# Kernel tuning notes

Hardware: AMD Instinct MI355X
Metric: run time of the kernel (lower is better)

Reference implementation:

```python
import jax, jax.numpy as jnp
import numpy as np

EPS = 1e-05  # epsilon from __init__
K, D = 2048, 256  # codebook_size, embed dim (hardcoded in module)
B, T = 8, 8192


def setup_inputs() -> dict:
    key = jax.random.key(0)
    k1, k2, k3 = jax.random.split(key, 3)
    hidden_states = jax.random.normal(k1, (B, T, D), dtype=jnp.float32)
    embed_sum = jax.random.normal(k2, (K, D), dtype=jnp.float32)
    # cluster_usage starts as ones in the module; use positive random counts
    cluster_usage = jax.random.uniform(k3, (K,), dtype=jnp.float32) * 10.0 + 0.5
    return {"hidden_states": hidden_states, "embed_sum": embed_sum, "cluster_usage": cluster_usage}


def reference(hidden_states, embed_sum, cluster_usage):
    # embed property: embed_sum / clamp(cluster_usage, min=eps)[:, None]
    embed = embed_sum / jnp.clip(cluster_usage, EPS, None)[:, None]  # [K, D]

    shape = hidden_states.shape
    x = hidden_states.reshape(-1, shape[-1]).astype(jnp.float32)  # [N, D]

    x2 = jnp.sum(x * x, axis=-1, keepdims=True)        # [N, 1]
    e2 = jnp.sum(embed * embed, axis=-1)               # [K]
    d2 = x2 - 2.0 * (x @ embed.T) + e2[None, :]        # [N, K] -- the big intermediate

    embed_ind = jnp.argmin(d2, axis=-1).reshape(shape[:-1])  # [B, T]
    # decode: embedding lookup of selected codes
    quantized = jnp.take(embed, embed_ind, axis=0)            # [B, T, D]
    return embed_ind, quantized
```

## Files before the change

### kernel.cpp

```cpp
#include <hip/hip_runtime.h>
#include <hip/hip_bf16.h>


typedef float f32x4 __attribute__((ext_vector_type(4)));
typedef short s16x8 __attribute__((ext_vector_type(8)));
typedef _Float16 h16x8 __attribute__((ext_vector_type(8)));

#define D_DIM 256
#define N_ROWS 65536
#define K_CODES 2048
#define VQ_EPS 1e-5f
#define DELTA 0.25f

__device__ __forceinline__ short f16s(float f) {
    _Float16 h = (_Float16)f;
    return __builtin_bit_cast(short, h);
}
__device__ __forceinline__ unsigned fkey(float f) {
    unsigned u = __float_as_uint(f);
    return u ^ (unsigned)(((int)u >> 31) | (int)0x80000000);
}
__device__ __forceinline__ float funkey(unsigned k) {
    unsigned u = (k & 0x80000000u) ? (k ^ 0x80000000u) : ~k;
    return __uint_as_float(u);
}
__device__ __forceinline__ void gload16(const void* g, void* l) {
    __builtin_amdgcn_global_load_lds(
        (const __attribute__((address_space(1))) void*)g,
        (__attribute__((address_space(3))) void*)l, 16, 0, 0);
}

__device__ __forceinline__ void np_sumsq_16lane(const float* a, float* out, int g) {
#pragma clang fp contract(off)
    int j = g & 7, h = g >> 3;
    const float* p = a + h * 128;
    float t = p[j];
    float r = t * t;
#pragma unroll
    for (int i = 1; i < 16; ++i) { float v = p[j + 8 * i]; r += v * v; }
    r += __shfl_xor(r, 1);
    r += __shfl_xor(r, 2);
    r += __shfl_xor(r, 4);
    float other = __shfl_xor(r, 8);
    if (g == 0) *out = r + other;
}

__global__ void prep_codebook(const float* __restrict__ es, const float* __restrict__ us,
                              float* __restrict__ embed, unsigned short* __restrict__ eswz,
                              float* __restrict__ e2) {
    __shared__ float le[8][256];
    const int tid = threadIdx.x;
    const int rloc = tid >> 5, idx = tid & 31;
    const int r = blockIdx.x * 8 + rloc;
    const float u = fmaxf(us[r], VQ_EPS);
    f32x4 v0 = *(const f32x4*)&es[r * D_DIM + idx * 8];
    f32x4 v1 = *(const f32x4*)&es[r * D_DIM + idx * 8 + 4];
    f32x4 e0, e1;
#pragma unroll
    for (int j = 0; j < 4; ++j) { e0[j] = v0[j] / u; e1[j] = v1[j] / u; }
    *(f32x4*)&embed[r * D_DIM + idx * 8] = e0;
    *(f32x4*)&embed[r * D_DIM + idx * 8 + 4] = e1;
    *(f32x4*)&le[rloc][idx * 8] = e0;
    *(f32x4*)&le[rloc][idx * 8 + 4] = e1;
    int kc = idx >> 2, ss = idx & 3;
    int sd = ss ^ ((r >> 1) & 3);
    s16x8 b;
#pragma unroll
    for (int j = 0; j < 4; ++j) { b[j] = f16s(e0[j]); b[j + 4] = f16s(e1[j]); }
    *(s16x8*)&eswz[r * 256 + kc * 32 + sd * 8] = b;
    __syncthreads();
    if (idx < 16) np_sumsq_16lane(&le[rloc][0], &e2[r], idx);
}

__global__ void prep_x(const float* __restrict__ x, unsigned short* __restrict__ dst,
                       float* __restrict__ x2) {
    int gid = blockIdx.x * 256 + threadIdx.x;
    int r = gid >> 5, idx = gid & 31;
    int kc = idx >> 2, s = idx & 3;
    int k0 = kc * 32 + (s ^ ((r >> 1) & 3)) * 8;
    const float* p = x + r * D_DIM + k0;
    s16x8 v;
#pragma unroll
    for (int j = 0; j < 8; ++j) v[j] = f16s(p[j]);
    *(s16x8*)&dst[r * 256 + kc * 32 + s * 8] = v;
    if (idx < 16)
        np_sumsq_16lane(x + r * D_DIM, x2 + r, idx);
}

__launch_bounds__(256, 2)
__global__ void vq_scan(const unsigned short* __restrict__ xswz,
                        const unsigned short* __restrict__ eswz,
                        const float* __restrict__ e2, const float* __restrict__ x2,
                        uint4* __restrict__ keys) {
    __shared__ __align__(16) short lds[2][2][4096];

    const int bid = blockIdx.x;
    const int swz = (bid & 7) * 1024 + (bid >> 3);
    const int mt = swz >> 4, nt = swz & 15;
    const int m_base = mt * 128, n_base = nt * 128;
    const int tid = threadIdx.x, lane = tid & 63, wid = tid >> 6;
    const int rb = wid * 32;
    const int l15 = lane & 15, lg = lane >> 4;

    f32x4 acc[2][8];
#pragma unroll
    for (int m = 0; m < 2; ++m)
#pragma unroll
        for (int n = 0; n < 8; ++n) { f32x4 z = {0.f, 0.f, 0.f, 0.f}; acc[m][n] = z; }

    auto stage = [&](int buf, int kc) {
#pragma unroll
        for (int i = 0; i < 2; ++i) {
            int off = i * 4096 + wid * 1024 + lane * 16;
            int row = off >> 6, slot = (off >> 4) & 3;
            gload16((const char*)xswz + (((size_t)(m_base + row)) << 9) + (kc << 6) + (slot << 4),
                    (char*)&lds[buf][0][0] + off);
            gload16((const char*)eswz + (((size_t)(n_base + row)) << 9) + (kc << 6) + (slot << 4),
                    (char*)&lds[buf][1][0] + off);
        }
    };
    auto compute = [&](int buf) {
        const short* A = &lds[buf][0][0];
        const short* B = &lds[buf][1][0];
        h16x8 af[2], bf[8];
#pragma unroll
        for (int m = 0; m < 2; ++m) {
            int R = rb + m * 16 + l15, s = lg ^ ((R >> 1) & 3);
            af[m] = __builtin_bit_cast(h16x8, *(const s16x8*)&A[R * 32 + s * 8]);
        }
#pragma unroll
        for (int n = 0; n < 8; ++n) {
            int R = n * 16 + l15, s = lg ^ ((R >> 1) & 3);
            bf[n] = __builtin_bit_cast(h16x8, *(const s16x8*)&B[R * 32 + s * 8]);
        }
#pragma unroll
        for (int m = 0; m < 2; ++m)
#pragma unroll
            for (int n = 0; n < 8; ++n)
                acc[m][n] = __builtin_amdgcn_mfma_f32_16x16x32_f16(af[m], bf[n], acc[m][n], 0, 0, 0);
    };

    stage(0, 0);
    __syncthreads();
#pragma unroll 1
    for (int kc = 0; kc < 8; ++kc) {
        if (kc < 7) stage((kc + 1) & 1, kc + 1);
        compute(kc & 1);
        __syncthreads();
    }

    const int grow0 = m_base + rb + lg * 4;
    float e2v[8];
#pragma unroll
    for (int n = 0; n < 8; ++n) e2v[n] = e2[n_base + n * 16 + l15];

#pragma unroll
    for (int m = 0; m < 2; ++m) {
#pragma unroll
        for (int j = 0; j < 4; ++j) {
            int gr = grow0 + m * 16 + j;
            float x2v = x2[gr];
            unsigned k1 = 0xFFFFFFFFu, k2 = 0xFFFFFFFFu;
            unsigned k3 = 0xFFFFFFFFu, k4 = 0xFFFFFFFFu;
#pragma unroll
            for (int n = 0; n < 8; ++n) {
                float d2 = (x2v - 2.0f * acc[m][n][j]) + e2v[n];
                unsigned pk = (fkey(d2) & 0xFFFFF800u)
                              | (unsigned)(n_base + n * 16 + l15);
                unsigned a = min(pk, k1), b = max(pk, k1); k1 = a;
                a = min(b, k2); b = max(b, k2); k2 = a;
                a = min(b, k3); b = max(b, k3); k3 = a;
                k4 = min(b, k4);
            }
#pragma unroll
            for (int s = 1; s < 16; s <<= 1) {
                unsigned o1 = __shfl_xor(k1, s), o2 = __shfl_xor(k2, s);
                unsigned o3 = __shfl_xor(k3, s), o4 = __shfl_xor(k4, s);
                unsigned c1 = min(k1, o4), c2 = min(k2, o3);
                unsigned c3 = min(k3, o2), c4 = min(k4, o1);
                unsigned t;
                t = min(c1, c3); c3 = max(c1, c3); c1 = t;
                t = min(c2, c4); c4 = max(c2, c4); c2 = t;
                t = min(c1, c2); c2 = max(c1, c2); c1 = t;
                t = min(c3, c4); c4 = max(c3, c4); c3 = t;
                k1 = c1; k2 = c2; k3 = c3; k4 = c4;
            }
            if (l15 == 0) {
                uint4 kq; kq.x = k1; kq.y = k2; kq.z = k3; kq.w = k4;
                keys[gr * 16 + nt] = kq;
            }
        }
    }
}

__launch_bounds__(256, 4)
__global__ void vq_rescore(const float* __restrict__ x, const float* __restrict__ embed,
                           const float* __restrict__ e2, const float* __restrict__ x2,
                           const uint4* __restrict__ keys,
                           const float* __restrict__ es, const float* __restrict__ us,
                           float* __restrict__ out) {
    __shared__ float lx[4][256];
    __shared__ float le[4][8][260];
    __shared__ int lcode[4][64];

    const int tid = threadIdx.x, w = tid >> 6, lane = tid & 63;
    const int r = blockIdx.x * 4 + w;
    const int t16 = lane & 15;
    const float x2v = x2[r];
    const unsigned long long lt = (1ull << lane) - 1ull;

    *(f32x4*)&lx[w][lane * 4] = *(const f32x4*)&x[r * D_DIM + lane * 4];

    uint4 kq = keys[r * 16 + t16];
    unsigned kmin = kq.x & 0xFFFFF800u;
#pragma unroll
    for (int s = 1; s < 16; s <<= 1) {
        unsigned ok = __shfl_xor(kmin, s);
        kmin = ok < kmin ? ok : kmin;
    }
    const float thr = funkey(kmin) + DELTA;

    unsigned sv[4] = {kq.x, kq.y, kq.z, kq.w};
    int nc = 0;
#pragma unroll
    for (int s = 0; s < 4; ++s) {
        bool v = (lane < 16) && (funkey(sv[s] & 0xFFFFF800u) <= thr);
        unsigned long long b = __ballot(v);
        if (v) lcode[w][nc + __popcll(b & lt)] = (int)(sv[s] & 0x7FFu);
        nc += (int)__popcll(b);
    }
    bool resc = (lane < 16) && (funkey(kq.w & 0xFFFFF800u) <= thr);
    unsigned long long rmask = __ballot(resc);

    float bv = __builtin_inff();
    int bi = 0x7FFFFFFF;
    auto lexmin = [&](float d2, int code) {
        if (d2 < bv || (d2 == bv && code < bi)) { bv = d2; bi = code; }
    };

#pragma unroll 1
    for (int g = 0; g < (nc + 7) >> 3; ++g) {
#pragma unroll
        for (int v = 0; v < 8; ++v) {
            int idx = g * 8 + v;
            if (idx < nc) {
                int code = lcode[w][idx];
                *(f32x4*)&le[w][v][lane * 4] =
                    *(const f32x4*)&embed[code * D_DIM + lane * 4];
            }
        }
        int idx = g * 8 + lane;
        if (lane < 8 && idx < nc) {
            int code = lcode[w][idx];
            float t = 0.0f;
#pragma unroll 8
            for (int k4 = 0; k4 < 64; ++k4) {
                f32x4 a4 = *(const f32x4*)&lx[w][k4 * 4];
                f32x4 e4 = *(const f32x4*)&le[w][lane][k4 * 4];
                t = __builtin_fmaf(a4[0], e4[0], t);
                t = __builtin_fmaf(a4[1], e4[1], t);
                t = __builtin_fmaf(a4[2], e4[2], t);
                t = __builtin_fmaf(a4[3], e4[3], t);
            }
            lexmin((x2v - 2.0f * t) + e2[code], code);
        }
    }

    while (rmask) {
        int t2 = __ffsll(rmask) - 1;
        rmask &= rmask - 1;
        int ca = t2 * 128 + lane, cb = ca + 64;
        float ta = 0.0f, tb = 0.0f;
#pragma unroll 8
        for (int k4 = 0; k4 < 64; ++k4) {
            f32x4 a4 = *(const f32x4*)&lx[w][k4 * 4];
            f32x4 ea = *(const f32x4*)&embed[ca * D_DIM + k4 * 4];
            f32x4 eb = *(const f32x4*)&embed[cb * D_DIM + k4 * 4];
            ta = __builtin_fmaf(a4[0], ea[0], ta);
            tb = __builtin_fmaf(a4[0], eb[0], tb);
            ta = __builtin_fmaf(a4[1], ea[1], ta);
            tb = __builtin_fmaf(a4[1], eb[1], tb);
            ta = __builtin_fmaf(a4[2], ea[2], ta);
            tb = __builtin_fmaf(a4[2], eb[2], tb);
            ta = __builtin_fmaf(a4[3], ea[3], ta);
            tb = __builtin_fmaf(a4[3], eb[3], tb);
        }
        lexmin((x2v - 2.0f * ta) + e2[ca], ca);
        lexmin((x2v - 2.0f * tb) + e2[cb], cb);
    }

#pragma unroll
    for (int s = 1; s < 64; s <<= 1) {
        float ov = __shfl_xor(bv, s);
        int oi = __shfl_xor(bi, s);
        if (ov < bv || (ov == bv && oi < bi)) { bv = ov; bi = oi; }
    }
    if (lane == 0) out[r] = (float)bi;

    float u = fmaxf(us[bi], VQ_EPS);
    f32x4 wv = *(const f32x4*)&es[bi * D_DIM + lane * 4];
    f32x4 o;
#pragma unroll
    for (int j = 0; j < 4; ++j) o[j] = wv[j] / u;
    *(f32x4*)&out[N_ROWS + r * D_DIM + lane * 4] = o;
}

extern "C" void kernel_launch(void* const* d_in, const int* in_sizes, int n_in,
                              void* d_out, int out_size, void* d_ws, size_t ws_size,
                              hipStream_t stream) {
    const float* x = (const float*)d_in[0];
    const float* es = (const float*)d_in[1];
    const float* us = (const float*)d_in[2];
    float* out = (float*)d_out;

    char* w = (char*)d_ws;
    unsigned short* xswz = (unsigned short*)(w);
    unsigned short* eswz = (unsigned short*)(w + 33554432);
    float* embed         = (float*)(w + 34603008);
    float* e2            = (float*)(w + 36700160);
    float* x2            = (float*)(w + 36708352);
    uint4* keys          = (uint4*)(w + 36970496);

    hipLaunchKernelGGL(prep_codebook, dim3(256), dim3(256), 0, stream,
                       es, us, embed, eswz, e2);
    hipLaunchKernelGGL(prep_x, dim3(8192), dim3(256), 0, stream, x, xswz, x2);
    hipLaunchKernelGGL(vq_scan, dim3(8192), dim3(256), 0, stream,
                       xswz, eswz, e2, x2, keys);
    hipLaunchKernelGGL(vq_rescore, dim3(16384), dim3(256), 0, stream,
                       x, embed, e2, x2, keys, es, us, out);
}
```

Measured before the change: 229.3 us.

## Make vq_scan persistent over codebook tiles with resident X tile in LDS

Each block now loads its 128-row X tile (all K chunks) into LDS once, then loops over all 16 codebook tiles, streaming B tiles through a double buffer. The grid shrinks from 8192 to 512 blocks. This removes the repeated reloading of the X tile for every codebook tile and the per-block prologue cost. In exchange, LDS use grows to about 80KB per block, which limits occupancy. With only 512 blocks there is less parallelism, and the epilogue is serialized inside the loop.

```diff
diff --git a/kernel.cpp b/kernel.cpp
--- a/kernel.cpp
+++ b/kernel.cpp
@@ -92,103 +92,115 @@
                         const unsigned short* __restrict__ eswz,
                         const float* __restrict__ e2, const float* __restrict__ x2,
                         uint4* __restrict__ keys) {
-    __shared__ __align__(16) short lds[2][2][4096];
-
-    const int bid = blockIdx.x;
-    const int swz = (bid & 7) * 1024 + (bid >> 3);
-    const int mt = swz >> 4, nt = swz & 15;
-    const int m_base = mt * 128, n_base = nt * 128;
+    __shared__ __align__(16) short lA[8][128][32];
+    __shared__ __align__(16) short lB[2][4096];
+
+    const int mt = blockIdx.x;
+    const int m_base = mt * 128;
     const int tid = threadIdx.x, lane = tid & 63, wid = tid >> 6;
     const int rb = wid * 32;
     const int l15 = lane & 15, lg = lane >> 4;
 
+#pragma unroll
+    for (int p = 0; p < 16; ++p) {
+        int off = p * 4096 + tid * 16;
+        int kc = off >> 13;
+        int w = off & 8191;
+        int row = w >> 6, slot = (w >> 4) & 3;
+        gload16((const char*)xswz + (((size_t)(m_base + row)) << 9) + (kc << 6) + (slot << 4),
+                (char*)&lA[0][0][0] + off);
+    }
+    auto stage_B = [&](int nt, int kc, int buf) {
+#pragma unroll
+        for (int i = 0; i < 2; ++i) {
+            int off = i * 4096 + tid * 16;
+            int row = off >> 6, slot = (off >> 4) & 3;
+            gload16((const char*)eswz + (((size_t)(nt * 128 + row)) << 9) + (kc << 6) + (slot << 4),
+                    (char*)&lB[buf][0] + off);
+        }
+    };
+    stage_B(0, 0, 0);
+    __syncthreads();
+
     f32x4 acc[2][8];
-#pragma unroll
-    for (int m = 0; m < 2; ++m)
-#pragma unroll
-        for (int n = 0; n < 8; ++n) { f32x4 z = {0.f, 0.f, 0.f, 0.f}; acc[m][n] = z; }
-
-    auto stage = [&](int buf, int kc) {
-#pragma unroll
-        for (int i = 0; i < 2; ++i) {
-            int off = i * 4096 + wid * 1024 + lane * 16;
-            int row = off >> 6, slot = (off >> 4) & 3;
-            gload16((const char*)xswz + (((size_t)(m_base + row)) << 9) + (kc << 6) + (slot << 4),
-                    (char*)&lds[buf][0][0] + off);
-            gload16((const char*)eswz + (((size_t)(n_base + row)) << 9) + (kc << 6) + (slot << 4),
-                    (char*)&lds[buf][1][0] + off);
-        }
-    };
-    auto compute = [&](int buf) {
-        const short* A = &lds[buf][0][0];
-        const short* B = &lds[buf][1][0];
-        h16x8 af[2], bf[8];
-#pragma unroll
-        for (int m = 0; m < 2; ++m) {
-            int R = rb + m * 16 + l15, s = lg ^ ((R >> 1) & 3);
-            af[m] = __builtin_bit_cast(h16x8, *(const s16x8*)&A[R * 32 + s * 8]);
-        }
-#pragma unroll
-        for (int n = 0; n < 8; ++n) {
-            int R = n * 16 + l15, s = lg ^ ((R >> 1) & 3);
-            bf[n] = __builtin_bit_cast(h16x8, *(const s16x8*)&B[R * 32 + s * 8]);
-        }
+    int buf = 0;
+#pragma unroll 1
+    for (int nt = 0; nt < 16; ++nt) {
+        const int n_base = nt * 128;
 #pragma unroll
         for (int m = 0; m < 2; ++m)
 #pragma unroll
-            for (int n = 0; n < 8; ++n)
-                acc[m][n] = __builtin_amdgcn_mfma_f32_16x16x32_f16(af[m], bf[n], acc[m][n], 0, 0, 0);
-    };
-
-    stage(0, 0);
-    __syncthreads();
+            for (int n = 0; n < 8; ++n) { f32x4 z = {0.f, 0.f, 0.f, 0.f}; acc[m][n] = z; }
+
 #pragma unroll 1
-    for (int kc = 0; kc < 8; ++kc) {
-        if (kc < 7) stage((kc + 1) & 1, kc + 1);
-        compute(kc & 1);
-        __syncthreads();
-    }
-
-    const int grow0 = m_base + rb + lg * 4;
-    float e2v[8];
-#pragma unroll
-    for (int n = 0; n < 8; ++n) e2v[n] = e2[n_base + n * 16 + l15];
-
-#pragma unroll
-    for (int m = 0; m < 2; ++m) {
-#pragma unroll
-        for (int j = 0; j < 4; ++j) {
-            int gr = grow0 + m * 16 + j;
-            float x2v = x2[gr];
-            unsigned k1 = 0xFFFFFFFFu, k2 = 0xFFFFFFFFu;
-            unsigned k3 = 0xFFFFFFFFu, k4 = 0xFFFFFFFFu;
-#pragma unroll
-            for (int n = 0; n < 8; ++n) {
-                float d2 = (x2v - 2.0f * acc[m][n][j]) + e2v[n];
-                unsigned pk = (fkey(d2) & 0xFFFFF800u)
-                              | (unsigned)(n_base + n * 16 + l15);
-                unsigned a = min(pk, k1), b = max(pk, k1); k1 = a;
-                a = min(b, k2); b = max(b, k2); k2 = a;
-                a = min(b, k3); b = max(b, k3); k3 = a;
-                k4 = min(b, k4);
+        for (int kc = 0; kc < 8; ++kc) {
+            int s = nt * 8 + kc;
+            if (s < 127) stage_B((s + 1) >> 3, (s + 1) & 7, buf ^ 1);
+            {
+                const short* A = &lA[kc][0][0];
+                const short* B = &lB[buf][0];
+                h16x8 af[2], bf[8];
+#pragma unroll
+                for (int m = 0; m < 2; ++m) {
+                    int R = rb + m * 16 + l15, sw = lg ^ ((R >> 1) & 3);
+                    af[m] = __builtin_bit_cast(h16x8, *(const s16x8*)&A[R * 32 + sw * 8]);
+                }
+#pragma unroll
+                for (int n = 0; n < 8; ++n) {
+                    int R = n * 16 + l15, sw = lg ^ ((R >> 1) & 3);
+                    bf[n] = __builtin_bit_cast(h16x8, *(const s16x8*)&B[R * 32 + sw * 8]);
+                }
+#pragma unroll
+                for (int m = 0; m < 2; ++m)
+#pragma unroll
+                    for (int n = 0; n < 8; ++n)
+                        acc[m][n] = __builtin_amdgcn_mfma_f32_16x16x32_f16(af[m], bf[n], acc[m][n], 0, 0, 0);
             }
-#pragma unroll
-            for (int s = 1; s < 16; s <<= 1) {
-                unsigned o1 = __shfl_xor(k1, s), o2 = __shfl_xor(k2, s);
-                unsigned o3 = __shfl_xor(k3, s), o4 = __shfl_xor(k4, s);
-                unsigned c1 = min(k1, o4), c2 = min(k2, o3);
-                unsigned c3 = min(k3, o2), c4 = min(k4, o1);
-                unsigned t;
-                t = min(c1, c3); c3 = max(c1, c3); c1 = t;
-                t = min(c2, c4); c4 = max(c2, c4); c2 = t;
-                t = min(c1, c2); c2 = max(c1, c2); c1 = t;
-                t = min(c3, c4); c4 = max(c3, c4); c3 = t;
-                k1 = c1; k2 = c2; k3 = c3; k4 = c4;
+            if (kc == 7) {
+                const int grow0 = m_base + rb + lg * 4;
+                float e2v[8];
+#pragma unroll
+                for (int n = 0; n < 8; ++n) e2v[n] = e2[n_base + n * 16 + l15];
+#pragma unroll
+                for (int m = 0; m < 2; ++m) {
+#pragma unroll
+                    for (int j = 0; j < 4; ++j) {
+                        int gr = grow0 + m * 16 + j;
+                        float x2v = x2[gr];
+                        unsigned k1 = 0xFFFFFFFFu, k2 = 0xFFFFFFFFu;
+                        unsigned k3 = 0xFFFFFFFFu, k4 = 0xFFFFFFFFu;
+#pragma unroll
+                        for (int n = 0; n < 8; ++n) {
+                            float d2 = (x2v - 2.0f * acc[m][n][j]) + e2v[n];
+                            unsigned pk = (fkey(d2) & 0xFFFFF800u)
+                                          | (unsigned)(n_base + n * 16 + l15);
+                            unsigned a = min(pk, k1), b = max(pk, k1); k1 = a;
+                            a = min(b, k2); b = max(b, k2); k2 = a;
+                            a = min(b, k3); b = max(b, k3); k3 = a;
+                            k4 = min(b, k4);
+                        }
+#pragma unroll
+                        for (int s2 = 1; s2 < 16; s2 <<= 1) {
+                            unsigned o1 = __shfl_xor(k1, s2), o2 = __shfl_xor(k2, s2);
+                            unsigned o3 = __shfl_xor(k3, s2), o4 = __shfl_xor(k4, s2);
+                            unsigned c1 = min(k1, o4), c2 = min(k2, o3);
+                            unsigned c3 = min(k3, o2), c4 = min(k4, o1);
+                            unsigned t;
+                            t = min(c1, c3); c3 = max(c1, c3); c1 = t;
+                            t = min(c2, c4); c4 = max(c2, c4); c2 = t;
+                            t = min(c1, c2); c2 = max(c1, c2); c1 = t;
+                            t = min(c3, c4); c4 = max(c3, c4); c3 = t;
+                            k1 = c1; k2 = c2; k3 = c3; k4 = c4;
+                        }
+                        if (l15 == 0) {
+                            uint4 kq; kq.x = k1; kq.y = k2; kq.z = k3; kq.w = k4;
+                            keys[gr * 16 + nt] = kq;
+                        }
+                    }
+                }
             }
-            if (l15 == 0) {
-                uint4 kq; kq.x = k1; kq.y = k2; kq.z = k3; kq.w = k4;
-                keys[gr * 16 + nt] = kq;
-            }
+            __syncthreads();
+            buf ^= 1;
         }
     }
 }
@@ -324,7 +336,7 @@
     hipLaunchKernelGGL(prep_codebook, dim3(256), dim3(256), 0, stream,
                        es, us, embed, eswz, e2);
     hipLaunchKernelGGL(prep_x, dim3(8192), dim3(256), 0, stream, x, xswz, x2);
-    hipLaunchKernelGGL(vq_scan, dim3(8192), dim3(256), 0, stream,
+    hipLaunchKernelGGL(vq_scan, dim3(512), dim3(256), 0, stream,
                        xswz, eswz, e2, x2, keys);
     hipLaunchKernelGGL(vq_rescore, dim3(16384), dim3(256), 0, stream,
                        x, embed, e2, x2, keys, es, us, out);
```

Result: slower. 272.3 us (+18.7%).

## Merge prep kernels, drop row-constant x2 from scan, use med3 top-4 insert

Applied to the files above, without the earlier changes.

Merges the codebook and x prep kernels into one launch split by block index, which removes a launch and lets the two kinds of work overlap. The scan stage now leaves out the per-row constant |x|^2 when ranking candidates, using fma(-2, dot, e2), so it no longer loads x2 and does less arithmetic. The top-4 insertion sort becomes one min plus three v_med3_u32 operations. Dropping x2 changes the key quantization that sets which candidates reach the rescore stage, which could alter tie and near-tie behaviour.

```diff
diff --git a/kernel.cpp b/kernel.cpp
--- a/kernel.cpp
+++ b/kernel.cpp
@@ -23,6 +23,11 @@
 __device__ __forceinline__ float funkey(unsigned k) {
     unsigned u = (k & 0x80000000u) ? (k ^ 0x80000000u) : ~k;
     return __uint_as_float(u);
+}
+__device__ __forceinline__ unsigned med3u(unsigned a, unsigned b, unsigned c) {
+    unsigned d;
+    asm("v_med3_u32 %0, %1, %2, %3" : "=v"(d) : "v"(a), "v"(b), "v"(c));
+    return d;
 }
 __device__ __forceinline__ void gload16(const void* g, void* l) {
     __builtin_amdgcn_global_load_lds(
@@ -45,52 +50,53 @@
     if (g == 0) *out = r + other;
 }
 
-__global__ void prep_codebook(const float* __restrict__ es, const float* __restrict__ us,
-                              float* __restrict__ embed, unsigned short* __restrict__ eswz,
-                              float* __restrict__ e2) {
+__global__ void prep_all(const float* __restrict__ es, const float* __restrict__ us,
+                         const float* __restrict__ x,
+                         float* __restrict__ embed, unsigned short* __restrict__ eswz,
+                         float* __restrict__ e2,
+                         unsigned short* __restrict__ xswz, float* __restrict__ x2) {
     __shared__ float le[8][256];
     const int tid = threadIdx.x;
-    const int rloc = tid >> 5, idx = tid & 31;
-    const int r = blockIdx.x * 8 + rloc;
-    const float u = fmaxf(us[r], VQ_EPS);
-    f32x4 v0 = *(const f32x4*)&es[r * D_DIM + idx * 8];
-    f32x4 v1 = *(const f32x4*)&es[r * D_DIM + idx * 8 + 4];
-    f32x4 e0, e1;
-#pragma unroll
-    for (int j = 0; j < 4; ++j) { e0[j] = v0[j] / u; e1[j] = v1[j] / u; }
-    *(f32x4*)&embed[r * D_DIM + idx * 8] = e0;
-    *(f32x4*)&embed[r * D_DIM + idx * 8 + 4] = e1;
-    *(f32x4*)&le[rloc][idx * 8] = e0;
-    *(f32x4*)&le[rloc][idx * 8 + 4] = e1;
-    int kc = idx >> 2, ss = idx & 3;
-    int sd = ss ^ ((r >> 1) & 3);
-    s16x8 b;
-#pragma unroll
-    for (int j = 0; j < 4; ++j) { b[j] = f16s(e0[j]); b[j + 4] = f16s(e1[j]); }
-    *(s16x8*)&eswz[r * 256 + kc * 32 + sd * 8] = b;
-    __syncthreads();
-    if (idx < 16) np_sumsq_16lane(&le[rloc][0], &e2[r], idx);
-}
-
-__global__ void prep_x(const float* __restrict__ x, unsigned short* __restrict__ dst,
-                       float* __restrict__ x2) {
-    int gid = blockIdx.x * 256 + threadIdx.x;
-    int r = gid >> 5, idx = gid & 31;
-    int kc = idx >> 2, s = idx & 3;
-    int k0 = kc * 32 + (s ^ ((r >> 1) & 3)) * 8;
-    const float* p = x + r * D_DIM + k0;
-    s16x8 v;
-#pragma unroll
-    for (int j = 0; j < 8; ++j) v[j] = f16s(p[j]);
-    *(s16x8*)&dst[r * 256 + kc * 32 + s * 8] = v;
-    if (idx < 16)
-        np_sumsq_16lane(x + r * D_DIM, x2 + r, idx);
+    if (blockIdx.x < 256) {
+        const int rloc = tid >> 5, idx = tid & 31;
+        const int r = blockIdx.x * 8 + rloc;
+        const float u = fmaxf(us[r], VQ_EPS);
+        f32x4 v0 = *(const f32x4*)&es[r * D_DIM + idx * 8];
+        f32x4 v1 = *(const f32x4*)&es[r * D_DIM + idx * 8 + 4];
+        f32x4 e0, e1;
+#pragma unroll
+        for (int j = 0; j < 4; ++j) { e0[j] = v0[j] / u; e1[j] = v1[j] / u; }
+        *(f32x4*)&embed[r * D_DIM + idx * 8] = e0;
+        *(f32x4*)&embed[r * D_DIM + idx * 8 + 4] = e1;
+        *(f32x4*)&le[rloc][idx * 8] = e0;
+        *(f32x4*)&le[rloc][idx * 8 + 4] = e1;
+        int kc = idx >> 2, ss = idx & 3;
+        int sd = ss ^ ((r >> 1) & 3);
+        s16x8 b;
+#pragma unroll
+        for (int j = 0; j < 4; ++j) { b[j] = f16s(e0[j]); b[j + 4] = f16s(e1[j]); }
+        *(s16x8*)&eswz[r * 256 + kc * 32 + sd * 8] = b;
+        __syncthreads();
+        if (idx < 16) np_sumsq_16lane(&le[rloc][0], &e2[r], idx);
+    } else {
+        int gid = (blockIdx.x - 256) * 256 + tid;
+        int r = gid >> 5, idx = gid & 31;
+        int kc = idx >> 2, s = idx & 3;
+        int k0 = kc * 32 + (s ^ ((r >> 1) & 3)) * 8;
+        const float* p = x + r * D_DIM + k0;
+        s16x8 v;
+#pragma unroll
+        for (int j = 0; j < 8; ++j) v[j] = f16s(p[j]);
+        *(s16x8*)&xswz[r * 256 + kc * 32 + s * 8] = v;
+        if (idx < 16)
+            np_sumsq_16lane(x + r * D_DIM, x2 + r, idx);
+    }
 }
 
 __launch_bounds__(256, 2)
 __global__ void vq_scan(const unsigned short* __restrict__ xswz,
                         const unsigned short* __restrict__ eswz,
-                        const float* __restrict__ e2, const float* __restrict__ x2,
+                        const float* __restrict__ e2,
                         uint4* __restrict__ keys) {
     __shared__ __align__(16) short lds[2][2][4096];
 
@@ -159,18 +165,18 @@
 #pragma unroll
         for (int j = 0; j < 4; ++j) {
             int gr = grow0 + m * 16 + j;
-            float x2v = x2[gr];
             unsigned k1 = 0xFFFFFFFFu, k2 = 0xFFFFFFFFu;
             unsigned k3 = 0xFFFFFFFFu, k4 = 0xFFFFFFFFu;
 #pragma unroll
             for (int n = 0; n < 8; ++n) {
-                float d2 = (x2v - 2.0f * acc[m][n][j]) + e2v[n];
-                unsigned pk = (fkey(d2) & 0xFFFFF800u)
+                float sv = __builtin_fmaf(-2.0f, acc[m][n][j], e2v[n]);
+                unsigned pk = (fkey(sv) & 0xFFFFF800u)
                               | (unsigned)(n_base + n * 16 + l15);
-                unsigned a = min(pk, k1), b = max(pk, k1); k1 = a;
-                a = min(b, k2); b = max(b, k2); k2 = a;
-                a = min(b, k3); b = max(b, k3); k3 = a;
-                k4 = min(b, k4);
+                unsigned n1 = min(pk, k1);
+                unsigned n2 = med3u(pk, k1, k2);
+                unsigned n3 = med3u(pk, k2, k3);
+                unsigned n4 = med3u(pk, k3, k4);
+                k1 = n1; k2 = n2; k3 = n3; k4 = n4;
             }
 #pragma unroll
             for (int s = 1; s < 16; s <<= 1) {
@@ -321,11 +327,10 @@
     float* x2            = (float*)(w + 36708352);
     uint4* keys          = (uint4*)(w + 36970496);
 
-    hipLaunchKernelGGL(prep_codebook, dim3(256), dim3(256), 0, stream,
-                       es, us, embed, eswz, e2);
-    hipLaunchKernelGGL(prep_x, dim3(8192), dim3(256), 0, stream, x, xswz, x2);
+    hipLaunchKernelGGL(prep_all, dim3(8448), dim3(256), 0, stream,
+                       es, us, x, embed, eswz, e2, xswz, x2);
     hipLaunchKernelGGL(vq_scan, dim3(8192), dim3(256), 0, stream,
-                       xswz, eswz, e2, x2, keys);
+                       xswz, eswz, e2, keys);
     hipLaunchKernelGGL(vq_rescore, dim3(16384), dim3(256), 0, stream,
                        x, embed, e2, x2, keys, es, us, out);
 }
```

Result: faster. 221.4 us (-3.4%).
